# Performance work log

Hardware: AMD Instinct MI355X
Metric: run time of the kernel (lower is better)

The kernel has to match this reference:

```python
import jax, jax.numpy as jnp
import numpy as np


def _layernorm(x, g, b, eps=1e-5):
    m = x.mean(-1, keepdims=True)
    v = ((x - m) ** 2).mean(-1, keepdims=True)
    return (x - m) * jax.lax.rsqrt(v + eps) * g + b


def _rmsnorm(x, w, eps=1e-6):
    return x * jax.lax.rsqrt((x * x).mean(-1, keepdims=True) + eps) * w


def setup_inputs() -> dict:
    key = jax.random.key(0)
    ks = jax.random.split(key, 8)
    B, T, S, C_img = 1, 3, 880, 3072
    C_mouse, D_hid, Dd = 2, 1024, 64
    vin = C_img + 12 * C_mouse  # 3096 = img_hidden + mouse_dim_in*vae_tcr*windows
    w = lambda k, shp: (jax.random.normal(k, shp, jnp.float32) * 0.02)
    return dict(
        x=jax.random.normal(ks[0], (B, T * S, C_img), jnp.float32),
        condition=jax.random.normal(ks[1], (B, 12, C_mouse), jnp.float32),
        w1=w(ks[2], (vin, D_hid)), b1=jnp.zeros((D_hid,), jnp.float32),
        w2=w(ks[3], (D_hid, D_hid)), b2=jnp.zeros((D_hid,), jnp.float32),
        ln_g=jnp.ones((D_hid,), jnp.float32), ln_b=jnp.zeros((D_hid,), jnp.float32),
        wqkv=w(ks[4], (D_hid, 3 * D_hid)), bqkv=jnp.zeros((3 * D_hid,), jnp.float32),
        qn_w=jnp.ones((Dd,), jnp.float32), kn_w=jnp.ones((Dd,), jnp.float32),
        wproj=w(ks[5], (D_hid, C_img)), bproj=jnp.zeros((C_img,), jnp.float32),
        H=22, W=40, temporal_shape=3, num_frame_per_block=3,
    )


def reference(x, condition, w1, b1, w2, b2, ln_g, ln_b, wqkv, bqkv,
              qn_w, kn_w, wproj, bproj, H, W, temporal_shape, num_frame_per_block):
    B, T_S, C_img = x.shape
    T = temporal_shape
    if condition.shape[1] > 9:
        condition = condition[:, -12:, :]
    _, N_frames, C = condition.shape
    action_len, pad_len = 20, 12
    pad = jnp.zeros((B, action_len - N_frames, C), condition.dtype)
    mouse_padded = jnp.concatenate([pad, condition], axis=1)  # [B, 20, C]
    # windowed gather: fixed small loop over num_frame_per_block (<=3)
    wins = jnp.stack([mouse_padded[:, i * 4:i * 4 + pad_len, :]
                      for i in range(num_frame_per_block)], axis=1)  # [B, F, 12, C]
    gm = wins.reshape(B, num_frame_per_block, pad_len * C)  # [B, F, 12C]
    S = 880  # hardcoded in original forward
    gm = jnp.broadcast_to(gm[:, None], (B, S, num_frame_per_block, pad_len * C))
    gm = gm.reshape(B * S, num_frame_per_block, pad_len * C)
    # fuse broadcast mouse features with image tokens (raw row-major reshape, as in torch)
    fused = jnp.concatenate([x.reshape(B * S, T, C_img), gm], axis=-1)  # [BS, T, C_img+12C]
    h = jax.nn.gelu(fused @ w1 + b1, approximate=True) @ w2 + b2
    h = _layernorm(h, ln_g, ln_b)  # [BS, T, D_hid]
    qkv = h @ wqkv + bqkv  # [BS, T, 3*D_hid]
    Dd = qn_w.shape[0]
    Hh = qkv.shape[-1] // (3 * Dd)
    qkv = qkv.reshape(B * S, T, 3, Hh, Dd)
    q, k, v = qkv[:, :, 0], qkv[:, :, 1], qkv[:, :, 2]
    q = _rmsnorm(q, qn_w).astype(v.dtype)
    k = _rmsnorm(k, kn_w).astype(v.dtype)
    # original flattens to one sequence of BS*T tokens for single_prefill (non-causal)
    N = B * S * T
    qf = q.reshape(N, Hh, Dd)
    kf = k.reshape(N, Hh, Dd)
    vf = v.reshape(N, Hh, Dd)
    scale = 1.0 / np.sqrt(Dd).astype(np.float32)
    scores = jnp.einsum('nhd,mhd->hnm', qf, kf) * scale  # [Hh, N, N]
    attn = jax.nn.softmax(scores, axis=-1)
    o = jnp.einsum('hnm,mhd->nhd', attn, vf)  # [N, Hh, Dd]
    # '(B S) T H D -> B (T S) (H D)'
    o = o.reshape(B, S, T, Hh, Dd).transpose(0, 2, 1, 3, 4).reshape(B, T * S, Hh * Dd)
    out = o @ wproj + bproj
    return x + out
```

## Files before the change

kernel.cpp:

```cpp
#include <hip/hip_runtime.h>
#include <hip/hip_bf16.h>

typedef __attribute__((ext_vector_type(8))) short short8;
typedef __attribute__((ext_vector_type(4))) short short4v;
typedef __attribute__((ext_vector_type(4))) unsigned uint4v;
typedef __attribute__((ext_vector_type(4))) float f32x4;
typedef __attribute__((ext_vector_type(16))) float f32x16;
typedef unsigned short u16;

#define ZERO16 (f32x16){0,0,0,0,0,0,0,0,0,0,0,0,0,0,0,0}

__device__ __forceinline__ float b2f(u16 h) {
    unsigned u = ((unsigned)h) << 16;
    float f; __builtin_memcpy(&f, &u, 4); return f;
}
__device__ __forceinline__ u16 f2b(float f) {
    __hip_bfloat16 h = __float2bfloat16(f);
    u16 r; __builtin_memcpy(&r, &h, 2); return r;
}
__device__ __forceinline__ void gload16(const void* g, void* l) {
    __builtin_amdgcn_global_load_lds(
        (const __attribute__((address_space(1))) unsigned*)g,
        (__attribute__((address_space(3))) unsigned*)l, 16, 0, 0);
}
__device__ __forceinline__ unsigned cvtpk_bf16(float lo, float hi) {
    unsigned d;
    asm("v_cvt_pk_bf16_f32 %0, %1, %2" : "=v"(d) : "v"(lo), "v"(hi));
    return d;
}

#define M_VALID 2640
#define M_PAD   2688
#define K1      3096
#define K1P     3136
#define DH      1024
#define CIMG    3072
#define NHEAD   16
#define NT      84
#define QTP     42
#define NSPLIT  3
#define TILES_PER_SPLIT 28
#define LOG2E   1.4426950408889634f

__global__ __launch_bounds__(256) void build_fused_kernel(
    const float* __restrict__ x, const float* __restrict__ cond,
    u16* __restrict__ fused)
{
    int n = blockIdx.x;
    int tid = threadIdx.x;
    const float* xr = x + (size_t)n * CIMG;
    u16* fr = fused + (size_t)n * K1P;
    for (int c = tid * 4; c < CIMG; c += 1024) {
        float4 v = *(const float4*)(xr + c);
        short4v w;
        w[0] = (short)f2b(v.x); w[1] = (short)f2b(v.y);
        w[2] = (short)f2b(v.z); w[3] = (short)f2b(v.w);
        *(short4v*)(fr + c) = w;
    }
    if (tid < 16) {
        int t = n % 3;
        short4v w;
        for (int jj = 0; jj < 4; jj++) {
            int j = tid * 4 + jj;
            float val = 0.f;
            if (j < 24) {
                int f = t * 4 + (j >> 1);
                if (f >= 8) val = cond[(f - 8) * 2 + (j & 1)];
            }
            w[jj] = (short)f2b(val);
        }
        *(short4v*)(fr + CIMG + tid * 4) = w;
    }
}

__global__ __launch_bounds__(256) void transpose_all_kernel(
    const float* __restrict__ w1, const float* __restrict__ w2,
    const float* __restrict__ wqkv, const float* __restrict__ wproj,
    u16* __restrict__ w1t, u16* __restrict__ w2t,
    u16* __restrict__ wqkvt, u16* __restrict__ wprojt)
{
    int b = blockIdx.x;
    const float* W; u16* Wt; int K, N, ldt, nx;
    if (b < 3136)      {            W = w1;    Wt = w1t;    K = K1; N = DH;   ldt = K1P; nx = 32; }
    else if (b < 4160) { b -= 3136; W = w2;    Wt = w2t;    K = DH; N = DH;   ldt = DH;  nx = 32; }
    else if (b < 7232) { b -= 4160; W = wqkv;  Wt = wqkvt;  K = DH; N = 3072; ldt = DH;  nx = 96; }
    else               { b -= 7232; W = wproj; Wt = wprojt; K = DH; N = CIMG; ldt = DH;  nx = 96; }
    __shared__ float t[32][33];
    int n0 = (b % nx) * 32, k0 = (b / nx) * 32;
    int x = threadIdx.x & 31, y0 = threadIdx.x >> 5;
    for (int yy = y0; yy < 32; yy += 8) {
        int k = k0 + yy, n = n0 + x;
        t[yy][x] = (k < K && n < N) ? W[(size_t)k * N + n] : 0.f;
    }
    __syncthreads();
    for (int yy = y0; yy < 32; yy += 8) {
        int n = n0 + yy, k = k0 + x;
        if (n < N && k < ldt) Wt[(size_t)n * ldt + k] = f2b(t[x][yy]);
    }
}

template<int EPI, int BM, int BN>
__global__ __launch_bounds__(256) void gemm_kernel(
    const u16* __restrict__ A, const u16* __restrict__ Bt,
    const float* __restrict__ bias, const float* __restrict__ resid,
    u16* __restrict__ Cb, float* __restrict__ Cf,
    int N, int K, int Mvalid)
{
    constexpr int MI  = BM / 32;
    constexpr int NJ  = BN / 32;
    constexpr int CA  = BM / 32;
    constexpr int CB  = BN / 32;
    constexpr unsigned ABYTES = BM * 128;
    constexpr unsigned BBYTES = BN * 128;
    constexpr unsigned STG = 2 * (ABYTES + BBYTES);
    constexpr unsigned CTW = BN + 4;
    constexpr unsigned CTB = BM * CTW * 4;
    constexpr int TPR = 256 / BM;
    __shared__ __align__(16) char smem[STG > CTB ? STG : CTB];

    const int tid = threadIdx.x;
    const int lane = tid & 63, wid = tid >> 6;
    const int l15 = lane & 15, l4 = lane >> 4;

    const int nx = N / BN;
    const int nwg = nx * (M_PAD / BM);
    const int bid = blockIdx.x;
    const int wgid = (bid & 7) * (nwg >> 3) + (bid >> 3);
    const int m0 = (wgid / nx) * BM, n0 = (wgid % nx) * BN;

    const int wr = (wid >> 1) * (BM / 2), wc = (wid & 1) * (BN / 2);

    const int srow = lane >> 3;
    const int scol = ((lane & 7) ^ (lane >> 3)) << 3;

    f32x4 acc[MI][NJ];
#pragma unroll
    for (int i = 0; i < MI; i++)
#pragma unroll
        for (int j = 0; j < NJ; j++) acc[i][j] = (f32x4){0.f, 0.f, 0.f, 0.f};

    const int nt = K >> 6;

    auto stage = [&](int buf, int k0) {
        char* Ab = smem + buf * ABYTES;
        char* Bb = smem + 2 * ABYTES + buf * BBYTES;
#pragma unroll
        for (int i = 0; i < CA; i++) {
            int c = wid * CA + i;
            gload16(A + (size_t)(m0 + c * 8 + srow) * K + k0 + scol,
                    Ab + c * 1024 + lane * 16);
        }
#pragma unroll
        for (int i = 0; i < CB; i++) {
            int c = wid * CB + i;
            gload16(Bt + (size_t)(n0 + c * 8 + srow) * K + k0 + scol,
                    Bb + c * 1024 + lane * 16);
        }
    };

    stage(0, 0);
    __syncthreads();
    int cur = 0;
    for (int t = 0; t < nt; t++) {
        if (t + 1 < nt) stage(cur ^ 1, (t + 1) * 64);
        const char* Ab = smem + cur * ABYTES;
        const char* Bb = smem + 2 * ABYTES + cur * BBYTES;
#pragma unroll
        for (int ki = 0; ki < 2; ki++) {
            short8 af[MI], bfr[NJ];
#pragma unroll
            for (int i = 0; i < MI; i++) {
                int row = wr + i * 16 + l15;
                af[i] = *(const short8*)(Ab + row * 128 + (((ki * 4 + l4) ^ (l15 & 7)) << 4));
            }
#pragma unroll
            for (int j = 0; j < NJ; j++) {
                int row = wc + j * 16 + l15;
                bfr[j] = *(const short8*)(Bb + row * 128 + (((ki * 4 + l4) ^ (l15 & 7)) << 4));
            }
            __builtin_amdgcn_s_setprio(1);
#pragma unroll
            for (int i = 0; i < MI; i++)
#pragma unroll
                for (int j = 0; j < NJ; j++)
                    acc[i][j] = __builtin_amdgcn_mfma_f32_16x16x32_bf16(af[i], bfr[j], acc[i][j], 0, 0, 0);
            __builtin_amdgcn_s_setprio(0);
        }
        __syncthreads();
        cur ^= 1;
    }

    float* Ct = (float*)smem;
#pragma unroll
    for (int i = 0; i < MI; i++)
#pragma unroll
        for (int j = 0; j < NJ; j++)
#pragma unroll
            for (int r = 0; r < 4; r++)
                Ct[(wr + i * 16 + l4 * 4 + r) * CTW + wc + j * 16 + l15] = acc[i][j][r];
    __syncthreads();

    const int row = tid / TPR;
    const int cb  = (tid % TPR) * (BN / TPR);
    const int grow = m0 + row;
    const int gcol = n0 + cb;
    if (EPI == 2) {
        if (grow < Mvalid) {
#pragma unroll
            for (int u = 0; u < BN / (4 * TPR); u++) {
                f32x4 v = *(const f32x4*)&Ct[row * CTW + cb + u * 4];
                float4 bv = *(const float4*)&bias[gcol + u * 4];
                float4 rv = *(const float4*)&resid[(size_t)grow * N + gcol + u * 4];
                float4 o;
                o.x = v[0] + bv.x + rv.x; o.y = v[1] + bv.y + rv.y;
                o.z = v[2] + bv.z + rv.z; o.w = v[3] + bv.w + rv.w;
                *(float4*)&Cf[(size_t)grow * N + gcol + u * 4] = o;
            }
        }
    } else {
        u16 tmp[BN / TPR];
#pragma unroll
        for (int u = 0; u < BN / (4 * TPR); u++) {
            f32x4 v = *(const f32x4*)&Ct[row * CTW + cb + u * 4];
            float4 bv = *(const float4*)&bias[gcol + u * 4];
#pragma unroll
            for (int e = 0; e < 4; e++) {
                float val = v[e] + ((const float*)&bv)[e];
                if (EPI == 0) {
                    float tt = val + 0.044715f * val * val * val;
                    val = 0.5f * val * (1.0f + tanhf(0.7978845608028654f * tt));
                }
                tmp[u * 4 + e] = f2b(val);
            }
        }
#pragma unroll
        for (int u = 0; u < BN / (8 * TPR); u++)
            *(short8*)(Cb + (size_t)grow * N + gcol + u * 8) = *(const short8*)&tmp[u * 8];
    }
}

__global__ __launch_bounds__(256) void ln_kernel(
    const u16* __restrict__ h2, const float* __restrict__ g,
    const float* __restrict__ b, u16* __restrict__ out)
{
    int row = blockIdx.x;
    int tid = threadIdx.x;
    const u16* p = h2 + (size_t)row * DH;
    float v[4];
#pragma unroll
    for (int i = 0; i < 4; i++) v[i] = b2f(p[tid * 4 + i]);
    float s1 = v[0] + v[1] + v[2] + v[3];
    float s2 = v[0]*v[0] + v[1]*v[1] + v[2]*v[2] + v[3]*v[3];
    for (int m = 1; m < 64; m <<= 1) { s1 += __shfl_xor(s1, m); s2 += __shfl_xor(s2, m); }
    __shared__ float a1[4], a2[4];
    int w = tid >> 6;
    if ((tid & 63) == 0) { a1[w] = s1; a2[w] = s2; }
    __syncthreads();
    s1 = a1[0] + a1[1] + a1[2] + a1[3];
    s2 = a2[0] + a2[1] + a2[2] + a2[3];
    float mean = s1 * (1.0f / 1024.0f);
    float var = s2 * (1.0f / 1024.0f) - mean * mean;
    float rs = rsqrtf(var + 1e-5f);
    u16* q = out + (size_t)row * DH;
#pragma unroll
    for (int i = 0; i < 4; i++) {
        int c = tid * 4 + i;
        q[c] = f2b((v[i] - mean) * rs * g[c] + b[c]);
    }
}

__global__ __launch_bounds__(256) void fragmentize_kernel(
    const u16* __restrict__ qkv, const float* __restrict__ qw, const float* __restrict__ kw,
    u16* __restrict__ Qf, u16* __restrict__ Kf, u16* __restrict__ Vf)
{
    __shared__ u16 Vlds[8 * 32 * 80];
    const int kt = blockIdx.x;
    const int hg = blockIdx.y;
    const int tid = threadIdx.x;
    const int t32 = tid >> 3, c8 = tid & 7;
    const int n = kt * 32 + t32;
    const u16* row = qkv + (size_t)n * 3072;

#pragma unroll
    for (int hh = 0; hh < 8; hh++) {
        short8 v = *(const short8*)(row + 2048 + (hg * 8 + hh) * 64 + c8 * 8);
        *(short8*)(&Vlds[(hh * 32 + t32) * 80 + c8 * 8]) = v;
    }

    float sq[8], sk[8];
#pragma unroll
    for (int hh = 0; hh < 8; hh++) {
        int h = hg * 8 + hh;
        short8 qv = *(const short8*)(row + h * 64 + c8 * 8);
        short8 kv = *(const short8*)(row + 1024 + h * 64 + c8 * 8);
        float aq = 0.f, ak = 0.f;
#pragma unroll
        for (int e = 0; e < 8; e++) {
            float fq = b2f((u16)qv[e]); aq += fq * fq;
            float fk = b2f((u16)kv[e]); ak += fk * fk;
        }
        sq[hh] = aq; sk[hh] = ak;
    }
#pragma unroll
    for (int m = 1; m < 8; m <<= 1) {
#pragma unroll
        for (int hh = 0; hh < 8; hh++) {
            sq[hh] += __shfl_xor(sq[hh], m);
            sk[hh] += __shfl_xor(sk[hh], m);
        }
    }

    float qwv[8], kwv[8];
#pragma unroll
    for (int e = 0; e < 8; e++) { qwv[e] = qw[c8 * 8 + e]; kwv[e] = kw[c8 * 8 + e]; }

#pragma unroll
    for (int hh = 0; hh < 8; hh++) {
        int h = hg * 8 + hh;
        float rq = rsqrtf(sq[hh] * (1.0f / 64.0f) + 1e-6f) * (0.125f * LOG2E);
        float rk = rsqrtf(sk[hh] * (1.0f / 64.0f) + 1e-6f);
        short8 qv = *(const short8*)(row + h * 64 + c8 * 8);
        short8 kv = *(const short8*)(row + 1024 + h * 64 + c8 * 8);
        short8 qo, ko;
#pragma unroll
        for (int e = 0; e < 8; e++) {
            qo[e] = (short)f2b(b2f((u16)qv[e]) * rq * qwv[e]);
            ko[e] = (short)f2b(b2f((u16)kv[e]) * rk * kwv[e]);
        }
        size_t base = (((size_t)(h * NT + kt) * 4 + (c8 >> 1)) << 9) + t32 * 16 + (c8 & 1) * 8;
        *(short8*)(Qf + base) = qo;
        *(short8*)(Kf + base) = ko;
    }

    __syncthreads();

    const int fd = tid >> 6;
    const int lkq = (tid & 63) >> 1, lhi = tid & 1;
#pragma unroll
    for (int hh = 0; hh < 8; hh++) {
        int h = hg * 8 + hh;
        short8 o;
#pragma unroll
        for (int e = 0; e < 8; e++)
            o[e] = (short)Vlds[(hh * 32 + (fd & 1) * 16 + lhi * 8 + e) * 80 + (fd >> 1) * 32 + lkq];
        *(short8*)(Vf + (((size_t)(h * NT + kt) * 4 + fd) << 9) + lkq * 16 + lhi * 8) = o;
    }
}

__device__ __forceinline__ void attn_tile(
    f32x16& st, float& lr, f32x16& o0, f32x16& o1, const short8* vv)
{
    float sum = 0.f;
    float p[16];
#pragma unroll
    for (int r = 0; r < 16; r++) { p[r] = __builtin_amdgcn_exp2f(st[r]); sum += p[r]; }
    lr += sum + __shfl_xor(sum, 32);

    unsigned a0 = cvtpk_bf16(p[0], p[1]),   a1 = cvtpk_bf16(p[2], p[3]);
    unsigned a2 = cvtpk_bf16(p[4], p[5]),   a3 = cvtpk_bf16(p[6], p[7]);
    unsigned a4 = cvtpk_bf16(p[8], p[9]),   a5 = cvtpk_bf16(p[10], p[11]);
    unsigned a6 = cvtpk_bf16(p[12], p[13]), a7 = cvtpk_bf16(p[14], p[15]);
    asm("v_permlane32_swap_b32 %0, %1" : "+v"(a0), "+v"(a2));
    asm("v_permlane32_swap_b32 %0, %1" : "+v"(a1), "+v"(a3));
    asm("v_permlane32_swap_b32 %0, %1" : "+v"(a4), "+v"(a6));
    asm("v_permlane32_swap_b32 %0, %1" : "+v"(a5), "+v"(a7));
    uint4v u0 = {a0, a1, a2, a3}, u1 = {a4, a5, a6, a7};
    short8 pa0, pa1;
    __builtin_memcpy(&pa0, &u0, 16);
    __builtin_memcpy(&pa1, &u1, 16);

    __builtin_amdgcn_s_setprio(1);
    o0 = __builtin_amdgcn_mfma_f32_32x32x16_bf16(pa0, vv[0], o0, 0, 0, 0);
    o0 = __builtin_amdgcn_mfma_f32_32x32x16_bf16(pa1, vv[1], o0, 0, 0, 0);
    o1 = __builtin_amdgcn_mfma_f32_32x32x16_bf16(pa0, vv[2], o1, 0, 0, 0);
    o1 = __builtin_amdgcn_mfma_f32_32x32x16_bf16(pa1, vv[3], o1, 0, 0, 0);
    __builtin_amdgcn_s_setprio(0);
}

__global__ __launch_bounds__(128, 4) void attn_kernel(
    const u16* __restrict__ Qf, const u16* __restrict__ Kf,
    const u16* __restrict__ Vf, u16* __restrict__ part, float* __restrict__ ml)
{
    const int bid = blockIdx.x;
    const int s   = bid / (NHEAD * QTP);
    const int rem = bid % (NHEAD * QTP);
    const int h   = rem / QTP;
    const int qtp = rem % QTP;
    const int wid = threadIdx.x >> 6;
    const int qt  = qtp * 2 + wid;
    const int lane = threadIdx.x & 63;
    const int kq = lane & 31;
    const int hi = lane >> 5;
    const int q0 = qt * 32;
    const int lxy = kq * 16 + hi * 8;
    const u16* Kh = Kf + ((size_t)h * NT * 4 << 9);
    const u16* Vh = Vf + ((size_t)h * NT * 4 << 9);

    short8 qf[4];
#pragma unroll
    for (int d = 0; d < 4; d++)
        qf[d] = *(const short8*)(Qf + (((size_t)(h * NT + qt) * 4 + d) << 9) + lxy);

    f32x16 o0 = ZERO16, o1 = ZERO16;
    float lr = 0.f;

    const int ts0 = s * TILES_PER_SPLIT;
    short8 kf[4];
#pragma unroll
    for (int d = 0; d < 4; d++)
        kf[d] = *(const short8*)(Kh + (((size_t)ts0 * 4 + d) << 9) + lxy);

    for (int i = 0; i < TILES_PER_SPLIT; i++) {
        const int tile = ts0 + i;
        const int k0 = tile * 32;
        short8 vv[4];
#pragma unroll
        for (int fd = 0; fd < 4; fd++)
            vv[fd] = *(const short8*)(Vh + (((size_t)tile * 4 + fd) << 9) + lxy);

        f32x16 st = ZERO16;
        __builtin_amdgcn_s_setprio(1);
#pragma unroll
        for (int d = 0; d < 4; d++)
            st = __builtin_amdgcn_mfma_f32_32x32x16_bf16(kf[d], qf[d], st, 0, 0, 0);
        __builtin_amdgcn_s_setprio(0);

        if (i < TILES_PER_SPLIT - 1) {
#pragma unroll
            for (int d = 0; d < 4; d++)
                kf[d] = *(const short8*)(Kh + (((size_t)(tile + 1) * 4 + d) << 9) + lxy);
        }

        if (k0 + 32 > M_VALID) {
#pragma unroll
            for (int r = 0; r < 16; r++) {
                int key = k0 + (r & 3) + 8 * (r >> 2) + 4 * hi;
                if (key >= M_VALID) st[r] = -3.0e38f;
            }
        }
        attn_tile(st, lr, o0, o1, vv);
    }

#pragma unroll
    for (int r = 0; r < 16; r++) {
        int rl = (r & 3) + 8 * (r >> 2) + 4 * hi;
        int qrow = q0 + rl;
        if (qrow < M_VALID) {
            u16* pp = part + ((size_t)s * M_PAD + qrow) * DH + h * 64;
            pp[kq] = f2b(o0[r]);
            pp[kq + 32] = f2b(o1[r]);
        }
    }
    if (hi == 0 && q0 + kq < M_VALID)
        ml[((size_t)s * NHEAD + h) * M_PAD + q0 + kq] = lr;
}

__global__ __launch_bounds__(256) void attn_merge_kernel(
    const u16* __restrict__ part, const float* __restrict__ ml, u16* __restrict__ obf)
{
    const int q = blockIdx.x;
    const int t = threadIdx.x;
    const int h = t >> 4, i = t & 15;
    float L = 0.f;
#pragma unroll
    for (int s = 0; s < NSPLIT; s++)
        L += ml[((size_t)s * NHEAD + h) * M_PAD + q];
    float inv = 1.0f / L;
    float4 acc = {0.f, 0.f, 0.f, 0.f};
#pragma unroll
    for (int s = 0; s < NSPLIT; s++) {
        short4v v = *(const short4v*)(part + ((size_t)s * M_PAD + q) * DH + h * 64 + i * 4);
        acc.x += b2f((u16)v[0]); acc.y += b2f((u16)v[1]);
        acc.z += b2f((u16)v[2]); acc.w += b2f((u16)v[3]);
    }
    int mrow = (q % 3) * 880 + q / 3;
    short4v w;
    w[0] = (short)f2b(acc.x * inv); w[1] = (short)f2b(acc.y * inv);
    w[2] = (short)f2b(acc.z * inv); w[3] = (short)f2b(acc.w * inv);
    *(short4v*)(obf + (size_t)mrow * DH + h * 64 + i * 4) = w;
}

extern "C" void kernel_launch(void* const* d_in, const int* in_sizes, int n_in,
                              void* d_out, int out_size, void* d_ws, size_t ws_size,
                              hipStream_t stream)
{
    const float* x      = (const float*)d_in[0];
    const float* cond   = (const float*)d_in[1];
    const float* w1     = (const float*)d_in[2];
    const float* b1     = (const float*)d_in[3];
    const float* w2     = (const float*)d_in[4];
    const float* b2     = (const float*)d_in[5];
    const float* ln_g   = (const float*)d_in[6];
    const float* ln_b   = (const float*)d_in[7];
    const float* wqkv   = (const float*)d_in[8];
    const float* bqkv   = (const float*)d_in[9];
    const float* qn_w   = (const float*)d_in[10];
    const float* kn_w   = (const float*)d_in[11];
    const float* wproj  = (const float*)d_in[12];
    const float* bproj  = (const float*)d_in[13];
    float* out = (float*)d_out;

    char* ws = (char*)d_ws;
    size_t off = 0;
    auto alloc = [&](size_t bytes) { size_t o = off; off += (bytes + 255) & ~(size_t)255; return o; };

    size_t off_fused  = alloc((size_t)M_PAD * K1P * 2);
    size_t off_w1t    = alloc((size_t)DH * K1P * 2);
    size_t off_w2t    = alloc((size_t)DH * DH * 2);
    size_t off_wqkvt  = alloc((size_t)3072 * DH * 2);
    size_t off_wprojt = alloc((size_t)CIMG * DH * 2);
    size_t off_h1     = alloc((size_t)M_PAD * DH * 2);
    size_t off_h2     = alloc((size_t)M_PAD * DH * 2);
    size_t off_h2ln   = alloc((size_t)M_PAD * DH * 2);
    size_t off_qkv    = alloc((size_t)M_PAD * 3072 * 2);
    size_t off_qf     = alloc((size_t)NHEAD * NT * 4 * 512 * 2);
    size_t off_kf     = alloc((size_t)NHEAD * NT * 4 * 512 * 2);
    size_t off_vf     = alloc((size_t)NHEAD * NT * 4 * 512 * 2);
    size_t off_obf    = alloc((size_t)M_PAD * DH * 2);
    (void)ws_size;

    u16* fused  = (u16*)(ws + off_fused);
    u16* w1t    = (u16*)(ws + off_w1t);
    u16* w2t    = (u16*)(ws + off_w2t);
    u16* wqkvt  = (u16*)(ws + off_wqkvt);
    u16* wprojt = (u16*)(ws + off_wprojt);
    u16* h1     = (u16*)(ws + off_h1);
    u16* h2     = (u16*)(ws + off_h2);
    u16* h2ln   = (u16*)(ws + off_h2ln);
    u16* qkvb   = (u16*)(ws + off_qkv);
    u16* Qf     = (u16*)(ws + off_qf);
    u16* Kf     = (u16*)(ws + off_kf);
    u16* Vf     = (u16*)(ws + off_vf);
    u16* obf    = (u16*)(ws + off_obf);
    u16* part   = (u16*)(ws + off_h1);
    float* mlbf = (float*)(ws + off_fused);

    hipMemsetAsync(ws + off_fused + (size_t)M_VALID * K1P * 2, 0, (size_t)(M_PAD - M_VALID) * K1P * 2, stream);

    build_fused_kernel<<<M_VALID, 256, 0, stream>>>(x, cond, fused);
    transpose_all_kernel<<<10304, 256, 0, stream>>>(w1, w2, wqkv, wproj, w1t, w2t, wqkvt, wprojt);

    gemm_kernel<0, 64, 64><<<dim3((DH / 64) * (M_PAD / 64)), 256, 0, stream>>>(fused, w1t, b1, nullptr, h1, nullptr, DH, K1P, M_PAD);
    gemm_kernel<1, 64, 64><<<dim3((DH / 64) * (M_PAD / 64)), 256, 0, stream>>>(h1, w2t, b2, nullptr, h2, nullptr, DH, DH, M_PAD);
    ln_kernel<<<M_PAD, 256, 0, stream>>>(h2, ln_g, ln_b, h2ln);
    gemm_kernel<1, 128, 128><<<dim3((3072 / 128) * (M_PAD / 128)), 256, 0, stream>>>(h2ln, wqkvt, bqkv, nullptr, qkvb, nullptr, 3072, DH, M_PAD);
    fragmentize_kernel<<<dim3(NT, 2), 256, 0, stream>>>(qkvb, qn_w, kn_w, Qf, Kf, Vf);
    attn_kernel<<<dim3(NSPLIT * NHEAD * QTP), 128, 0, stream>>>(Qf, Kf, Vf, part, mlbf);
    attn_merge_kernel<<<M_VALID, 256, 0, stream>>>(part, mlbf, obf);
    gemm_kernel<2, 128, 128><<<dim3((CIMG / 128) * (M_PAD / 128)), 256, 0, stream>>>(obf, wprojt, bproj, x, nullptr, out, CIMG, DH, M_VALID);
}
```

Baseline: 188.7 us.

## Software-pipeline attention loop to overlap QK^T MFMA with softmax-PV of previous tile

```diff
diff --git a/kernel.cpp b/kernel.cpp
--- a/kernel.cpp
+++ b/kernel.cpp
@@ -377,7 +377,7 @@
     __builtin_amdgcn_s_setprio(0);
 }
 
-__global__ __launch_bounds__(128, 4) void attn_kernel(
+__global__ __launch_bounds__(128, 3) void attn_kernel(
     const u16* __restrict__ Qf, const u16* __restrict__ Kf,
     const u16* __restrict__ Vf, u16* __restrict__ part, float* __restrict__ ml)
 {
@@ -403,34 +403,28 @@
 
     f32x16 o0 = ZERO16, o1 = ZERO16;
     float lr = 0.f;
-
     const int ts0 = s * TILES_PER_SPLIT;
-    short8 kf[4];
-#pragma unroll
-    for (int d = 0; d < 4; d++)
-        kf[d] = *(const short8*)(Kh + (((size_t)ts0 * 4 + d) << 9) + lxy);
-
-    for (int i = 0; i < TILES_PER_SPLIT; i++) {
-        const int tile = ts0 + i;
-        const int k0 = tile * 32;
+
+    auto loadK = [&](short8* k, int tile) {
+#pragma unroll
+        for (int d = 0; d < 4; d++)
+            k[d] = *(const short8*)(Kh + (((size_t)tile * 4 + d) << 9) + lxy);
+    };
+    auto qk = [&](const short8* k) {
+        f32x16 st = ZERO16;
+        __builtin_amdgcn_s_setprio(1);
+#pragma unroll
+        for (int d = 0; d < 4; d++)
+            st = __builtin_amdgcn_mfma_f32_32x32x16_bf16(k[d], qf[d], st, 0, 0, 0);
+        __builtin_amdgcn_s_setprio(0);
+        return st;
+    };
+    auto smpv = [&](f32x16& st, int tile) {
         short8 vv[4];
 #pragma unroll
         for (int fd = 0; fd < 4; fd++)
             vv[fd] = *(const short8*)(Vh + (((size_t)tile * 4 + fd) << 9) + lxy);
-
-        f32x16 st = ZERO16;
-        __builtin_amdgcn_s_setprio(1);
-#pragma unroll
-        for (int d = 0; d < 4; d++)
-            st = __builtin_amdgcn_mfma_f32_32x32x16_bf16(kf[d], qf[d], st, 0, 0, 0);
-        __builtin_amdgcn_s_setprio(0);
-
-        if (i < TILES_PER_SPLIT - 1) {
-#pragma unroll
-            for (int d = 0; d < 4; d++)
-                kf[d] = *(const short8*)(Kh + (((size_t)(tile + 1) * 4 + d) << 9) + lxy);
-        }
-
+        const int k0 = tile * 32;
         if (k0 + 32 > M_VALID) {
 #pragma unroll
             for (int r = 0; r < 16; r++) {
@@ -439,6 +433,22 @@
             }
         }
         attn_tile(st, lr, o0, o1, vv);
+    };
+
+    short8 kA[4], kB[4];
+    loadK(kA, ts0);
+    loadK(kB, ts0 + 1);
+    f32x16 stA = qk(kA);
+
+    for (int p = 0; p < TILES_PER_SPLIT / 2; p++) {
+        const int tA = ts0 + 2 * p;
+        f32x16 stB = qk(kB);
+        if (p < TILES_PER_SPLIT / 2 - 1) loadK(kA, tA + 2);
+        smpv(stA, tA);
+        f32x16 stA2 = ZERO16;
+        if (p < TILES_PER_SPLIT / 2 - 1) { stA2 = qk(kA); loadK(kB, tA + 3); }
+        smpv(stB, tA + 1);
+        stA = stA2;
     }
 
 #pragma unroll
```

After: 191.5 us. Within noise of the previous version (+1.5%).
